# Kernel optimization log

Measured on AMD Instinct MI355X. Metric: run time of the kernel, lower is better.

The kernel has to match this reference:

```python
import jax, jax.numpy as jnp
import numpy as np

DIM = 768
HEADS = 12
HD = DIM // HEADS
SCALE = HD ** -0.5


def setup_inputs() -> dict:
    key = jax.random.key(0)
    ks = jax.random.split(key, 12)
    B, N = 2, 2048
    s = DIM ** -0.5
    return {
        "x1": jax.random.normal(ks[0], (B, N, DIM), jnp.float32),
        "x2": jax.random.normal(ks[1], (B, N, DIM), jnp.float32),
        "Wq": jax.random.normal(ks[2], (DIM, DIM), jnp.float32) * s,
        "bq": jax.random.normal(ks[3], (DIM,), jnp.float32) * 0.01,
        "Wk": jax.random.normal(ks[4], (DIM, DIM), jnp.float32) * s,
        "bk": jax.random.normal(ks[5], (DIM,), jnp.float32) * 0.01,
        "Wv": jax.random.normal(ks[6], (DIM, DIM), jnp.float32) * s,
        "bv": jax.random.normal(ks[7], (DIM,), jnp.float32) * 0.01,
        "Wo": jax.random.normal(ks[8], (DIM, DIM), jnp.float32) * s,
        "bo": jax.random.normal(ks[9], (DIM,), jnp.float32) * 0.01,
        "cross_scale": jnp.array([0.5], jnp.float32),
    }


def _heads(x, W, b):
    # torch Linear: x @ W.T + b; then (B,N,H,hd) -> (B,H,N,hd)
    B, N, _ = x.shape
    y = x @ W.T + b
    return y.reshape(B, N, HEADS, HD).transpose(0, 2, 1, 3)


def reference(x1, x2, Wq, bq, Wk, bk, Wv, bv, Wo, bo, cross_scale):
    B, N, C = x1.shape
    q1, k1, v1 = _heads(x1, Wq, bq), _heads(x1, Wk, bk), _heads(x1, Wv, bv)
    q2, k2, v2 = _heads(x2, Wq, bq), _heads(x2, Wk, bk), _heads(x2, Wv, bv)

    s = cross_scale[0]
    attn11 = jnp.einsum('bhqd,bhkd->bhqk', q1, k1) * SCALE
    attn22 = jnp.einsum('bhqd,bhkd->bhqk', q2, k2) * SCALE
    attn12 = jnp.einsum('bhqd,bhkd->bhqk', q1, k2) * SCALE
    attn21 = jnp.einsum('bhqd,bhkd->bhqk', q2, k1) * SCALE

    a1 = jax.nn.softmax((1.0 - s) * attn11 + s * attn12, axis=-1)
    a2 = jax.nn.softmax((1.0 - s) * attn22 + s * attn21, axis=-1)

    o1 = jnp.einsum('bhqk,bhkd->bhqd', a1, v1).transpose(0, 2, 1, 3).reshape(B, N, C)
    o2 = jnp.einsum('bhqk,bhkd->bhqd', a2, v2).transpose(0, 2, 1, 3).reshape(B, N, C)

    out1 = o1 @ Wo.T + bo
    out2 = o2 @ Wo.T + bo
    return out1, out2
```

## Files before the change

kernel.cpp:

```cpp
#include <hip/hip_runtime.h>

#define KDIM 768
#define HALF 3145728
#define XAELEMS 6291456
#define WELEMS 589824
#define QS 0.18033688f

typedef __attribute__((ext_vector_type(8))) short short8;
typedef __attribute__((ext_vector_type(4))) short short4_;
typedef __attribute__((ext_vector_type(4))) float float4_;
typedef __attribute__((ext_vector_type(2))) unsigned int uint2_;

__device__ __forceinline__ unsigned short f2bf(float f) {
  unsigned int u = __float_as_uint(f);
  u += 0x7fffu + ((u >> 16) & 1u);
  return (unsigned short)(u >> 16);
}

__device__ __forceinline__ unsigned int pack2bf(float a, float b) {
  unsigned int ua = __float_as_uint(a) + 0x8000u;
  unsigned int ub = __float_as_uint(b) + 0x8000u;
  return __builtin_amdgcn_perm(ub, ua, 0x07060302);
}

__device__ __forceinline__ void gll16(const void* g, void* l) {
  __builtin_amdgcn_global_load_lds(
      (const __attribute__((address_space(1))) unsigned int*)g,
      (__attribute__((address_space(3))) unsigned int*)l, 16, 0, 0);
}

#if __has_builtin(__builtin_amdgcn_mfma_f32_16x16x16bf16_1k)
__device__ __forceinline__ float4_ mfma16(short4_ a, short4_ b, float4_ c) {
  return __builtin_amdgcn_mfma_f32_16x16x16bf16_1k(a, b, c, 0, 0, 0);
}
#else
__device__ __forceinline__ float4_ mfma16(short4_ a, short4_ b, float4_ c) {
  asm volatile("v_mfma_f32_16x16x16_bf16 %0, %1, %2, %0\n\ts_nop 7\n\ts_nop 7"
               : "+v"(c) : "v"(a), "v"(b));
  return c;
}
#endif

__global__ void prep_x_kernel(const float* __restrict__ x1, const float* __restrict__ x2,
                              const float* __restrict__ cs,
                              unsigned short* __restrict__ xa, unsigned short* __restrict__ xb) {
  const int i = (blockIdx.x * 256 + threadIdx.x) * 4;
  const float s = cs[0], t_ = 1.0f - s;
  float4 a = *(const float4*)(x1 + i);
  float4 b = *(const float4*)(x2 + i);
  ushort4 ua = { f2bf(a.x), f2bf(a.y), f2bf(a.z), f2bf(a.w) };
  ushort4 ub = { f2bf(b.x), f2bf(b.y), f2bf(b.z), f2bf(b.w) };
  *(ushort4*)(xa + i) = ua;
  *(ushort4*)(xa + HALF + i) = ub;
  ushort4 c1 = { f2bf(t_*a.x + s*b.x), f2bf(t_*a.y + s*b.y), f2bf(t_*a.z + s*b.z), f2bf(t_*a.w + s*b.w) };
  ushort4 c2 = { f2bf(t_*b.x + s*a.x), f2bf(t_*b.y + s*a.y), f2bf(t_*b.z + s*a.z), f2bf(t_*b.w + s*a.w) };
  *(ushort4*)(xb + i) = c1;
  *(ushort4*)(xb + HALF + i) = c2;
}

__global__ void conv_w4_kernel(const float* __restrict__ w0, const float* __restrict__ w1,
                               const float* __restrict__ w2, const float* __restrict__ w3,
                               unsigned short* __restrict__ o0, unsigned short* __restrict__ o1,
                               unsigned short* __restrict__ o2, unsigned short* __restrict__ o3) {
  const int z = blockIdx.y;
  const float* w = (z == 0) ? w0 : (z == 1) ? w1 : (z == 2) ? w2 : w3;
  unsigned short* o = (z == 0) ? o0 : (z == 1) ? o1 : (z == 2) ? o2 : o3;
  const int i = (blockIdx.x * 256 + threadIdx.x) * 4;
  float4 a = *(const float4*)(w + i);
  ushort4 ua = { f2bf(a.x), f2bf(a.y), f2bf(a.z), f2bf(a.w) };
  *(ushort4*)(o + i) = ua;
}

__device__ __forceinline__ void gemm_mainloop(const unsigned short* __restrict__ A,
                                              const unsigned short* __restrict__ W,
                                              unsigned short* As, unsigned short* Bs,
                                              int m0, int n0, int t, float4_ (&acc)[4][4]) {
  const int lane = t & 63, quad = lane >> 4, lrow = lane & 15;
  const int wave = t >> 6;
  const int wm = (wave & 1) * 64, wn = (wave >> 1) * 64;
  for (int kt = 0; kt < KDIM; kt += 64) {
#pragma unroll
    for (int i = 0; i < 4; i++) {
      const int li = i * 256 + t;
      const int row = li >> 3, cc = (li & 7) * 8;
      gll16(A + (size_t)(m0 + row) * KDIM + kt + cc, As + li * 8);
      gll16(W + (size_t)(n0 + row) * KDIM + kt + cc, Bs + li * 8);
    }
    __syncthreads();
#pragma unroll
    for (int kk = 0; kk < 2; kk++) {
      short8 af[4], bfr[4];
#pragma unroll
      for (int i = 0; i < 4; i++)
        af[i] = *(const short8*)(As + (wm + i * 16 + lrow) * 64 + kk * 32 + quad * 8);
#pragma unroll
      for (int j = 0; j < 4; j++)
        bfr[j] = *(const short8*)(Bs + (wn + j * 16 + lrow) * 64 + kk * 32 + quad * 8);
#pragma unroll
      for (int i = 0; i < 4; i++)
#pragma unroll
        for (int j = 0; j < 4; j++)
          acc[i][j] = __builtin_amdgcn_mfma_f32_16x16x32_bf16(af[i], bfr[j], acc[i][j], 0, 0, 0);
    }
    __syncthreads();
  }
}

__global__ __launch_bounds__(256, 2)
void qkv_gemm(const unsigned short* __restrict__ xa, const unsigned short* __restrict__ xb,
              const unsigned short* __restrict__ wq, const unsigned short* __restrict__ wk,
              const unsigned short* __restrict__ wv,
              const float* __restrict__ bq, const float* __restrict__ bk, const float* __restrict__ bv,
              unsigned short* __restrict__ qo, unsigned short* __restrict__ ko,
              unsigned short* __restrict__ vto) {
  __shared__ __align__(16) unsigned short smem[16384];
  unsigned short* As = smem;
  unsigned short* Bs = smem + 8192;
  const int t = threadIdx.x;
  const int z = blockIdx.z;
  const int m0 = blockIdx.x * 128, n0 = blockIdx.y * 128;
  const unsigned short* A = (z == 1) ? xb : xa;
  const unsigned short* W = (z == 0) ? wq : (z == 1) ? wk : wv;
  const float* bias = (z == 0) ? bq : (z == 1) ? bk : bv;
  float4_ acc[4][4];
#pragma unroll
  for (int i = 0; i < 4; i++)
#pragma unroll
    for (int j = 0; j < 4; j++) acc[i][j] = (float4_){0.f, 0.f, 0.f, 0.f};
  gemm_mainloop(A, W, As, Bs, m0, n0, t, acc);

  const int lane = t & 63, quad = lane >> 4, lrow = lane & 15;
  const int wave = t >> 6;
  const int wm = (wave & 1) * 64, wn = (wave >> 1) * 64;

  if (z == 2) {
    unsigned short* Tb = smem + wave * 4096;
#pragma unroll
    for (int i = 0; i < 4; i++) {
#pragma unroll
      for (int j = 0; j < 4; j++) {
        const int nl = j * 16 + lrow;
        const float bn = bias[n0 + wn + nl];
#pragma unroll
        for (int r = 0; r < 4; r++) {
          const int ml = i * 16 + quad * 4 + r;
          const int c = ml >> 3;
          Tb[nl * 64 + ((c ^ (nl & 7)) * 8) + (ml & 7)] = f2bf(acc[i][j][r] + bn);
        }
      }
    }
    __asm__ __volatile__("s_waitcnt lgkmcnt(0)");
    const int sb = (m0 + wm) >> 11;
    const int hh = (n0 + wn) >> 6;
    const int tokbase = ((m0 + wm) & 2047);
#pragma unroll
    for (int i3 = 0; i3 < 8; i3++) {
      const int ci = i3 * 64 + lane;
      const int row = ci >> 3, p = ci & 7;
      short8 rd = *(const short8*)(Tb + row * 64 + p * 8);
      const int c = p ^ (row & 7);
      *(short8*)(vto + ((size_t)(sb * 12 + hh) * 64 + row) * 2048 + tokbase + c * 8) = rd;
    }
  } else {
    unsigned short* dst = (z == 0) ? qo : ko;
    const float scale = (z == 0) ? QS : 1.0f;
#pragma unroll
    for (int i = 0; i < 4; i++) {
#pragma unroll
      for (int j = 0; j < 4; j++) {
        const int n = n0 + wn + j * 16 + lrow;
        const float bn = bias[n];
#pragma unroll
        for (int r = 0; r < 4; r++) {
          const int m = m0 + wm + i * 16 + quad * 4 + r;
          dst[(size_t)m * KDIM + n] = f2bf((acc[i][j][r] + bn) * scale);
        }
      }
    }
  }
}

__global__ __launch_bounds__(256, 2)
void out_gemm(const unsigned short* __restrict__ ob, const unsigned short* __restrict__ wo,
              const float* __restrict__ bo, float* __restrict__ out) {
  __shared__ __align__(16) unsigned short As[128 * 64];
  __shared__ __align__(16) unsigned short Bs[128 * 64];
  const int t = threadIdx.x;
  const int m0 = blockIdx.x * 128, n0 = blockIdx.y * 128;
  float4_ acc[4][4];
#pragma unroll
  for (int i = 0; i < 4; i++)
#pragma unroll
    for (int j = 0; j < 4; j++) acc[i][j] = (float4_){0.f, 0.f, 0.f, 0.f};
  gemm_mainloop(ob, wo, As, Bs, m0, n0, t, acc);

  const int lane = t & 63, quad = lane >> 4, lrow = lane & 15;
  const int wave = t >> 6;
  const int wm = (wave & 1) * 64, wn = (wave >> 1) * 64;
#pragma unroll
  for (int i = 0; i < 4; i++) {
#pragma unroll
    for (int j = 0; j < 4; j++) {
      const int n = n0 + wn + j * 16 + lrow;
      const float bn = bo[n];
#pragma unroll
      for (int r = 0; r < 4; r++) {
        const int m = m0 + wm + i * 16 + quad * 4 + r;
        out[(size_t)m * KDIM + n] = acc[i][j][r] + bn;
      }
    }
  }
}

__global__ __launch_bounds__(256, 2)
void attn_kernel(const unsigned short* __restrict__ qg, const unsigned short* __restrict__ kg,
                 const unsigned short* __restrict__ vt, unsigned short* __restrict__ o) {
  __shared__ __align__(16) unsigned short Ks[2][64 * 64];
  __shared__ __align__(16) unsigned short Vs[2][64 * 64];
  const int prob = blockIdx.x % 48;
  const int q0 = (blockIdx.x / 48) * 128;
  const int sb = prob / 12, h = prob % 12;
  const int t = threadIdx.x, w = t >> 6, lane = t & 63, quad = lane >> 4, lrow = lane & 15;
  const int mbase = sb * 2048;
  const size_t vbase = (size_t)prob * (64 * 2048);

  short8 bq[2][2];
#pragma unroll
  for (int i = 0; i < 2; i++) {
    const unsigned short* qp = qg + (size_t)(mbase + q0 + w * 32 + i * 16 + lrow) * KDIM + h * 64 + quad * 8;
    bq[i][0] = *(const short8*)qp;
    bq[i][1] = *(const short8*)(qp + 32);
  }
  float l_part[2] = {0.f, 0.f};
  float4_ oa[2][4];
#pragma unroll
  for (int i = 0; i < 2; i++)
#pragma unroll
    for (int d = 0; d < 4; d++) oa[i][d] = (float4_){0.f, 0.f, 0.f, 0.f};

  auto stage = [&](int k0, int b) {
#pragma unroll
    for (int i2 = 0; i2 < 2; i2++) {
      const int li = i2 * 256 + t;
      const int row = li >> 3, p = li & 7;
      const int c = p ^ (row & 7);
      gll16(kg + (size_t)(mbase + k0 + row) * KDIM + h * 64 + c * 8, &Ks[b][li * 8]);
    }
#pragma unroll
    for (int i2 = 0; i2 < 2; i2++) {
      const int li = i2 * 256 + t;
      const int row = li >> 3, p = li & 7;
      const int c = p ^ (row & 7);
      gll16(vt + vbase + (size_t)row * 2048 + k0 + c * 8, &Vs[b][li * 8]);
    }
  };
  stage(0, 0);

  for (int kt = 0; kt < 32; kt++) {
    __syncthreads();
    const int b = kt & 1;
    if (kt + 1 < 32) stage((kt + 1) * 64, b ^ 1);

    float4_ st[4][2];
#pragma unroll
    for (int nt = 0; nt < 4; nt++)
#pragma unroll
      for (int i = 0; i < 2; i++) st[nt][i] = (float4_){0.f, 0.f, 0.f, 0.f};
#pragma unroll
    for (int kk = 0; kk < 2; kk++) {
#pragma unroll
      for (int nt = 0; nt < 4; nt++) {
        short8 ak = *(const short8*)(&Ks[b][(nt * 16 + lrow) * 64 + (((kk * 4 + quad) ^ (lrow & 7)) * 8)]);
        st[nt][0] = __builtin_amdgcn_mfma_f32_16x16x32_bf16(ak, bq[0][kk], st[nt][0], 0, 0, 0);
        st[nt][1] = __builtin_amdgcn_mfma_f32_16x16x32_bf16(ak, bq[1][kk], st[nt][1], 0, 0, 0);
      }
    }

    short4_ pb[2][4];
#pragma unroll
    for (int nt = 0; nt < 4; nt++)
#pragma unroll
      for (int i = 0; i < 2; i++) {
        const float p0 = __builtin_amdgcn_exp2f(st[nt][i][0]);
        const float p1 = __builtin_amdgcn_exp2f(st[nt][i][1]);
        const float p2 = __builtin_amdgcn_exp2f(st[nt][i][2]);
        const float p3 = __builtin_amdgcn_exp2f(st[nt][i][3]);
        l_part[i] += (p0 + p1) + (p2 + p3);
        uint2_ uu = { pack2bf(p0, p1), pack2bf(p2, p3) };
        pb[i][nt] = __builtin_bit_cast(short4_, uu);
      }

#pragma unroll
    for (int nt = 0; nt < 4; nt++) {
      const int cp = (((nt * 2 + (quad >> 1)) ^ (lrow & 7)) * 8) + (quad & 1) * 4;
#pragma unroll
      for (int dt = 0; dt < 4; dt++) {
        short4_ av = *(const short4_*)(&Vs[b][(dt * 16 + lrow) * 64 + cp]);
        oa[0][dt] = mfma16(av, pb[0][nt], oa[0][dt]);
        oa[1][dt] = mfma16(av, pb[1][nt], oa[1][dt]);
      }
    }
  }

#pragma unroll
  for (int i = 0; i < 2; i++) {
    float l = l_part[i];
    l += __shfl_xor(l, 16);
    l += __shfl_xor(l, 32);
    const float inv = 1.0f / l;
    const size_t m = (size_t)mbase + q0 + w * 32 + i * 16 + lrow;
#pragma unroll
    for (int dt = 0; dt < 4; dt++) {
      uint2_ uu = { pack2bf(oa[i][dt][0] * inv, oa[i][dt][1] * inv),
                    pack2bf(oa[i][dt][2] * inv, oa[i][dt][3] * inv) };
      *(uint2_*)(o + m * KDIM + h * 64 + dt * 16 + quad * 4) = uu;
    }
  }
}

extern "C" void kernel_launch(void* const* d_in, const int* in_sizes, int n_in,
                              void* d_out, int out_size, void* d_ws, size_t ws_size,
                              hipStream_t stream) {
  const float* x1 = (const float*)d_in[0];
  const float* x2 = (const float*)d_in[1];
  const float* Wq = (const float*)d_in[2];
  const float* bq = (const float*)d_in[3];
  const float* Wk = (const float*)d_in[4];
  const float* bk = (const float*)d_in[5];
  const float* Wv = (const float*)d_in[6];
  const float* bv = (const float*)d_in[7];
  const float* Wo = (const float*)d_in[8];
  const float* bo = (const float*)d_in[9];
  const float* cs = (const float*)d_in[10];
  float* out = (float*)d_out;

  char* ws = (char*)d_ws;
  size_t off = 0;
  auto alloc = [&](size_t bytes) {
    void* p = ws + off;
    off += (bytes + 255) & ~(size_t)255;
    return p;
  };
  unsigned short* xa  = (unsigned short*)alloc((size_t)XAELEMS * 2);
  unsigned short* xb  = (unsigned short*)alloc((size_t)XAELEMS * 2);
  unsigned short* wqb = (unsigned short*)alloc((size_t)WELEMS * 2);
  unsigned short* wkb = (unsigned short*)alloc((size_t)WELEMS * 2);
  unsigned short* wvb = (unsigned short*)alloc((size_t)WELEMS * 2);
  unsigned short* wob = (unsigned short*)alloc((size_t)WELEMS * 2);
  unsigned short* qg  = (unsigned short*)alloc((size_t)XAELEMS * 2);
  unsigned short* kgb = (unsigned short*)alloc((size_t)XAELEMS * 2);
  unsigned short* vtb = (unsigned short*)alloc((size_t)XAELEMS * 2);
  unsigned short* ob  = (unsigned short*)alloc((size_t)XAELEMS * 2);

  prep_x_kernel<<<HALF / 1024, 256, 0, stream>>>(x1, x2, cs, xa, xb);
  conv_w4_kernel<<<dim3(WELEMS / 1024, 4), 256, 0, stream>>>(Wq, Wk, Wv, Wo, wqb, wkb, wvb, wob);
  qkv_gemm<<<dim3(64, 6, 3), 256, 0, stream>>>(xa, xb, wqb, wkb, wvb, bq, bk, bv, qg, kgb, vtb);
  attn_kernel<<<48 * 16, 256, 0, stream>>>(qg, kgb, vtb, ob);
  out_gemm<<<dim3(64, 6), 256, 0, stream>>>(ob, wob, bo, out);
}
```

Measured before the change: 226.6 us.

## Drop LDS staging in attention, read K/V directly; coalesce Q/K stores via LDS

```diff
diff --git a/kernel.cpp b/kernel.cpp
--- a/kernel.cpp
+++ b/kernel.cpp
@@ -164,18 +164,29 @@
   } else {
     unsigned short* dst = (z == 0) ? qo : ko;
     const float scale = (z == 0) ? QS : 1.0f;
+    unsigned short* Tb = smem + wave * 4096;
 #pragma unroll
     for (int i = 0; i < 4; i++) {
 #pragma unroll
       for (int j = 0; j < 4; j++) {
-        const int n = n0 + wn + j * 16 + lrow;
-        const float bn = bias[n];
+        const int nl = j * 16 + lrow;
+        const float bn = bias[n0 + wn + nl];
+        const int clog = nl >> 3, lo = nl & 7;
 #pragma unroll
         for (int r = 0; r < 4; r++) {
-          const int m = m0 + wm + i * 16 + quad * 4 + r;
-          dst[(size_t)m * KDIM + n] = f2bf((acc[i][j][r] + bn) * scale);
+          const int ml = i * 16 + quad * 4 + r;
+          Tb[ml * 64 + ((clog ^ (ml & 7)) * 8) + lo] = f2bf((acc[i][j][r] + bn) * scale);
         }
       }
+    }
+    __asm__ __volatile__("s_waitcnt lgkmcnt(0)");
+#pragma unroll
+    for (int i3 = 0; i3 < 8; i3++) {
+      const int ci = i3 * 64 + lane;
+      const int ml = ci >> 3, p = ci & 7;
+      short8 rd = *(const short8*)(Tb + ml * 64 + p * 8);
+      const int clog = p ^ (ml & 7);
+      *(short8*)(dst + (size_t)(m0 + wm + ml) * KDIM + n0 + wn + clog * 8) = rd;
     }
   }
 }
@@ -212,107 +223,81 @@
   }
 }
 
-__global__ __launch_bounds__(256, 2)
+__global__ __launch_bounds__(128, 2)
 void attn_kernel(const unsigned short* __restrict__ qg, const unsigned short* __restrict__ kg,
                  const unsigned short* __restrict__ vt, unsigned short* __restrict__ o) {
-  __shared__ __align__(16) unsigned short Ks[2][64 * 64];
-  __shared__ __align__(16) unsigned short Vs[2][64 * 64];
   const int prob = blockIdx.x % 48;
   const int q0 = (blockIdx.x / 48) * 128;
   const int sb = prob / 12, h = prob % 12;
   const int t = threadIdx.x, w = t >> 6, lane = t & 63, quad = lane >> 4, lrow = lane & 15;
   const int mbase = sb * 2048;
   const size_t vbase = (size_t)prob * (64 * 2048);
-
-  short8 bq[2][2];
-#pragma unroll
-  for (int i = 0; i < 2; i++) {
-    const unsigned short* qp = qg + (size_t)(mbase + q0 + w * 32 + i * 16 + lrow) * KDIM + h * 64 + quad * 8;
-    bq[i][0] = *(const short8*)qp;
-    bq[i][1] = *(const short8*)(qp + 32);
-  }
-  float l_part[2] = {0.f, 0.f};
-  float4_ oa[2][4];
-#pragma unroll
-  for (int i = 0; i < 2; i++)
-#pragma unroll
-    for (int d = 0; d < 4; d++) oa[i][d] = (float4_){0.f, 0.f, 0.f, 0.f};
-
-  auto stage = [&](int k0, int b) {
-#pragma unroll
-    for (int i2 = 0; i2 < 2; i2++) {
-      const int li = i2 * 256 + t;
-      const int row = li >> 3, p = li & 7;
-      const int c = p ^ (row & 7);
-      gll16(kg + (size_t)(mbase + k0 + row) * KDIM + h * 64 + c * 8, &Ks[b][li * 8]);
-    }
-#pragma unroll
-    for (int i2 = 0; i2 < 2; i2++) {
-      const int li = i2 * 256 + t;
-      const int row = li >> 3, p = li & 7;
-      const int c = p ^ (row & 7);
-      gll16(vt + vbase + (size_t)row * 2048 + k0 + c * 8, &Vs[b][li * 8]);
-    }
-  };
-  stage(0, 0);
+  const unsigned short* kb = kg + (size_t)mbase * KDIM + h * 64;
+
+  short8 bq[4][2];
+#pragma unroll
+  for (int qf = 0; qf < 4; qf++) {
+    const unsigned short* qp = qg + (size_t)(mbase + q0 + w * 64 + qf * 16 + lrow) * KDIM + h * 64 + quad * 8;
+    bq[qf][0] = *(const short8*)qp;
+    bq[qf][1] = *(const short8*)(qp + 32);
+  }
+  float l_part[4] = {0.f, 0.f, 0.f, 0.f};
+  float4_ oa[4][4];
+#pragma unroll
+  for (int qf = 0; qf < 4; qf++)
+#pragma unroll
+    for (int d = 0; d < 4; d++) oa[qf][d] = (float4_){0.f, 0.f, 0.f, 0.f};
 
   for (int kt = 0; kt < 32; kt++) {
-    __syncthreads();
-    const int b = kt & 1;
-    if (kt + 1 < 32) stage((kt + 1) * 64, b ^ 1);
-
-    float4_ st[4][2];
-#pragma unroll
-    for (int nt = 0; nt < 4; nt++)
-#pragma unroll
-      for (int i = 0; i < 2; i++) st[nt][i] = (float4_){0.f, 0.f, 0.f, 0.f};
-#pragma unroll
-    for (int kk = 0; kk < 2; kk++) {
-#pragma unroll
-      for (int nt = 0; nt < 4; nt++) {
-        short8 ak = *(const short8*)(&Ks[b][(nt * 16 + lrow) * 64 + (((kk * 4 + quad) ^ (lrow & 7)) * 8)]);
-        st[nt][0] = __builtin_amdgcn_mfma_f32_16x16x32_bf16(ak, bq[0][kk], st[nt][0], 0, 0, 0);
-        st[nt][1] = __builtin_amdgcn_mfma_f32_16x16x32_bf16(ak, bq[1][kk], st[nt][1], 0, 0, 0);
-      }
-    }
-
-    short4_ pb[2][4];
-#pragma unroll
-    for (int nt = 0; nt < 4; nt++)
-#pragma unroll
-      for (int i = 0; i < 2; i++) {
-        const float p0 = __builtin_amdgcn_exp2f(st[nt][i][0]);
-        const float p1 = __builtin_amdgcn_exp2f(st[nt][i][1]);
-        const float p2 = __builtin_amdgcn_exp2f(st[nt][i][2]);
-        const float p3 = __builtin_amdgcn_exp2f(st[nt][i][3]);
-        l_part[i] += (p0 + p1) + (p2 + p3);
+    const int k0 = kt * 64;
+#pragma unroll
+    for (int nt = 0; nt < 4; nt++) {
+      const unsigned short* kp = kb + (size_t)(k0 + nt * 16 + lrow) * KDIM + quad * 8;
+      short8 ak0 = *(const short8*)kp;
+      short8 ak1 = *(const short8*)(kp + 32);
+      float4_ st[4];
+#pragma unroll
+      for (int qf = 0; qf < 4; qf++)
+        st[qf] = __builtin_amdgcn_mfma_f32_16x16x32_bf16(ak0, bq[qf][0], (float4_){0.f,0.f,0.f,0.f}, 0, 0, 0);
+#pragma unroll
+      for (int qf = 0; qf < 4; qf++)
+        st[qf] = __builtin_amdgcn_mfma_f32_16x16x32_bf16(ak1, bq[qf][1], st[qf], 0, 0, 0);
+
+      short4_ pb[4];
+#pragma unroll
+      for (int qf = 0; qf < 4; qf++) {
+        const float p0 = __builtin_amdgcn_exp2f(st[qf][0]);
+        const float p1 = __builtin_amdgcn_exp2f(st[qf][1]);
+        const float p2 = __builtin_amdgcn_exp2f(st[qf][2]);
+        const float p3 = __builtin_amdgcn_exp2f(st[qf][3]);
+        l_part[qf] += (p0 + p1) + (p2 + p3);
         uint2_ uu = { pack2bf(p0, p1), pack2bf(p2, p3) };
-        pb[i][nt] = __builtin_bit_cast(short4_, uu);
-      }
-
-#pragma unroll
-    for (int nt = 0; nt < 4; nt++) {
-      const int cp = (((nt * 2 + (quad >> 1)) ^ (lrow & 7)) * 8) + (quad & 1) * 4;
+        pb[qf] = __builtin_bit_cast(short4_, uu);
+      }
+
 #pragma unroll
       for (int dt = 0; dt < 4; dt++) {
-        short4_ av = *(const short4_*)(&Vs[b][(dt * 16 + lrow) * 64 + cp]);
-        oa[0][dt] = mfma16(av, pb[0][nt], oa[0][dt]);
-        oa[1][dt] = mfma16(av, pb[1][nt], oa[1][dt]);
-      }
-    }
-  }
-
-#pragma unroll
-  for (int i = 0; i < 2; i++) {
-    float l = l_part[i];
+        const unsigned short* vp = vt + vbase + (size_t)(dt * 16 + lrow) * 2048 + k0 + nt * 16 + quad * 4;
+        short4_ av = *(const short4_*)vp;
+#pragma unroll
+        for (int qf = 0; qf < 4; qf++)
+          oa[qf][dt] = mfma16(av, pb[qf], oa[qf][dt]);
+      }
+    }
+    asm volatile("s_barrier" ::: "memory");
+  }
+
+#pragma unroll
+  for (int qf = 0; qf < 4; qf++) {
+    float l = l_part[qf];
     l += __shfl_xor(l, 16);
     l += __shfl_xor(l, 32);
     const float inv = 1.0f / l;
-    const size_t m = (size_t)mbase + q0 + w * 32 + i * 16 + lrow;
+    const size_t m = (size_t)mbase + q0 + w * 64 + qf * 16 + lrow;
 #pragma unroll
     for (int dt = 0; dt < 4; dt++) {
-      uint2_ uu = { pack2bf(oa[i][dt][0] * inv, oa[i][dt][1] * inv),
-                    pack2bf(oa[i][dt][2] * inv, oa[i][dt][3] * inv) };
+      uint2_ uu = { pack2bf(oa[qf][dt][0] * inv, oa[qf][dt][1] * inv),
+                    pack2bf(oa[qf][dt][2] * inv, oa[qf][dt][3] * inv) };
       *(uint2_*)(o + m * KDIM + h * 64 + dt * 16 + quad * 4) = uu;
     }
   }
@@ -355,6 +340,6 @@
   prep_x_kernel<<<HALF / 1024, 256, 0, stream>>>(x1, x2, cs, xa, xb);
   conv_w4_kernel<<<dim3(WELEMS / 1024, 4), 256, 0, stream>>>(Wq, Wk, Wv, Wo, wqb, wkb, wvb, wob);
   qkv_gemm<<<dim3(64, 6, 3), 256, 0, stream>>>(xa, xb, wqb, wkb, wvb, bq, bk, bv, qg, kgb, vtb);
-  attn_kernel<<<48 * 16, 256, 0, stream>>>(qg, kgb, vtb, ob);
+  attn_kernel<<<48 * 16, 128, 0, stream>>>(qg, kgb, vtb, ob);
   out_gemm<<<dim3(64, 6), 256, 0, stream>>>(ob, wob, bo, out);
 }
```

Result: slower. 298.3 us (+31.7%).
